# Kernel tuning notes

Hardware: AMD Instinct MI355X
Metric: run time of the kernel (lower is better)

Reference implementation:

```python
import jax, jax.numpy as jnp
import numpy as np

D_MODEL = 768
NHEAD = 12
D_K = D_MODEL // NHEAD
D_FF = 3072
EPS = 1e-6


def layer_norm(x, a, b):
    # torch LayerNorm here: mean/std over last dim, std is UNBIASED (n-1), eps added to std
    n = x.shape[-1]
    m = jnp.mean(x, axis=-1, keepdims=True)
    var = jnp.sum((x - m) ** 2, axis=-1, keepdims=True) / (n - 1)
    return a * (x - m) / (jnp.sqrt(var) + EPS) + b


def setup_inputs() -> dict:
    key = jax.random.key(0)
    ks = jax.random.split(key, 12)
    B, S = 2, 2048
    s = 1.0 / np.sqrt(D_MODEL)
    inp = {
        'x': jax.random.normal(ks[0], (B, S, D_MODEL), jnp.float32),
        'mask': jnp.ones((B, 1, S), jnp.int32),
        'Wq': jax.random.normal(ks[1], (D_MODEL, D_MODEL), jnp.float32) * s,
        'bq': jnp.zeros((D_MODEL,), jnp.float32),
        'Wk': jax.random.normal(ks[2], (D_MODEL, D_MODEL), jnp.float32) * s,
        'bk': jnp.zeros((D_MODEL,), jnp.float32),
        'Wv': jax.random.normal(ks[3], (D_MODEL, D_MODEL), jnp.float32) * s,
        'bv': jnp.zeros((D_MODEL,), jnp.float32),
        'Wo': jax.random.normal(ks[4], (D_MODEL, D_MODEL), jnp.float32) * s,
        'bo': jnp.zeros((D_MODEL,), jnp.float32),
        'ln1_a': jnp.ones((D_MODEL,), jnp.float32),
        'ln1_b': jnp.zeros((D_MODEL,), jnp.float32),
        'W1': jax.random.normal(ks[5], (D_MODEL, D_FF), jnp.float32) * s,
        'b1': jnp.zeros((D_FF,), jnp.float32),
        'W2': jax.random.normal(ks[6], (D_FF, D_MODEL), jnp.float32) * (1.0 / np.sqrt(D_FF)),
        'b2': jnp.zeros((D_MODEL,), jnp.float32),
        'ln2_a': jnp.ones((D_MODEL,), jnp.float32),
        'ln2_b': jnp.zeros((D_MODEL,), jnp.float32),
    }
    return inp


def reference(x, mask, Wq, bq, Wk, bk, Wv, bv, Wo, bo, ln1_a, ln1_b, W1, b1, W2, b2, ln2_a, ln2_b):
    B, S, _ = x.shape
    # --- sublayer 1: pre-norm self-attention + residual (dropout = eval/no-op) ---
    h = layer_norm(x, ln1_a, ln1_b)
    q = (h @ Wq + bq).reshape(B, S, NHEAD, D_K).transpose(0, 2, 1, 3)  # [B,H,S,Dk]
    k = (h @ Wk + bk).reshape(B, S, NHEAD, D_K).transpose(0, 2, 1, 3)
    v = (h @ Wv + bv).reshape(B, S, NHEAD, D_K).transpose(0, 2, 1, 3)
    scores = jnp.einsum('bhqd,bhkd->bhqk', q, k) / np.sqrt(D_K)  # [B,H,S,S]
    scores = jnp.where(mask[:, None] == 0, jnp.float32(-1e9), scores)
    attn = jax.nn.softmax(scores, axis=-1)
    ctx = jnp.einsum('bhqk,bhkd->bhqd', attn, v)  # [B,H,S,Dk]
    ctx = ctx.transpose(0, 2, 1, 3).reshape(B, S, D_MODEL)
    x = x + (ctx @ Wo + bo)
    # --- sublayer 2: pre-norm FFN + residual ---
    h2 = layer_norm(x, ln2_a, ln2_b)
    ff = jax.nn.relu(h2 @ W1 + b1) @ W2 + b2
    return x + ff
```

## Files before the change

kernel.cpp:

```cpp
#include <hip/hip_runtime.h>
#include <hip/hip_bf16.h>
#include <stdint.h>

#define DM 768
#define DFF 3072
#define NH 12
#define DK 64
#define SS 2048
#define NTOK 4096
#define KCH 2

typedef __hip_bfloat16 bf16;
typedef short bf16x8 __attribute__((ext_vector_type(8)));
typedef float f32x4 __attribute__((ext_vector_type(4)));

#define MFMA16(a, b, c) __builtin_amdgcn_mfma_f32_16x16x32_bf16((a), (b), (c), 0, 0, 0)

#define QSCALE 0.18033688011112042f

#if __has_builtin(__builtin_amdgcn_exp2f)
#define EXP2F(x) __builtin_amdgcn_exp2f(x)
#else
#define EXP2F(x) exp2f(x)
#endif

static __device__ __forceinline__ bf16 f2b(float f) { return __float2bfloat16(f); }
static __device__ __forceinline__ unsigned short f2b_bits(float f) {
    bf16 h = __float2bfloat16(f);
    return *reinterpret_cast<unsigned short*>(&h);
}
static __device__ __forceinline__ float b2f(bf16 h) { return __bfloat162float(h); }

static __device__ __forceinline__ void g2l16(const void* g, void* l) {
    __builtin_amdgcn_global_load_lds(
        (const __attribute__((address_space(1))) unsigned int*)g,
        (__attribute__((address_space(3))) unsigned int*)(uintptr_t)l,
        16, 0, 0);
}

__global__ __launch_bounds__(256) void transpose_all(const float* Wq, const float* Wk,
                                                     const float* Wv, const float* Wo,
                                                     const float* W1, const float* W2,
                                                     bf16* WqT, bf16* WkT, bf16* WvT,
                                                     bf16* WoT, bf16* W1T, bf16* W2T) {
    __shared__ float tile[32][33];
    int id = blockIdx.x;
    const float* W; bf16* WT; int K, N, n0, k0;
    if (id < 2304) {
        int z = id / 576, r = id % 576;
        W  = (z == 0) ? Wq : (z == 1) ? Wk : (z == 2) ? Wv : Wo;
        WT = (z == 0) ? WqT : (z == 1) ? WkT : (z == 2) ? WvT : WoT;
        K = 768; N = 768; n0 = (r % 24) * 32; k0 = (r / 24) * 32;
    } else if (id < 4608) {
        int r = id - 2304; W = W1; WT = W1T;
        K = 768; N = 3072; n0 = (r % 96) * 32; k0 = (r / 96) * 32;
    } else {
        int r = id - 4608; W = W2; WT = W2T;
        K = 3072; N = 768; n0 = (r % 24) * 32; k0 = (r / 24) * 32;
    }
    int tx = threadIdx.x & 31, ty = threadIdx.x >> 5;
#pragma unroll
    for (int r = ty; r < 32; r += 8)
        tile[r][tx] = W[(size_t)(k0 + r) * N + n0 + tx];
    __syncthreads();
#pragma unroll
    for (int r = ty; r < 32; r += 8)
        WT[(size_t)(n0 + r) * K + k0 + tx] = f2b(tile[tx][r]);
}

__global__ __launch_bounds__(256) void ln_fwd(const float* __restrict__ x,
                                              const float* __restrict__ g,
                                              const float* __restrict__ be,
                                              bf16* __restrict__ out) {
    int wid = threadIdx.x >> 6, lane = threadIdx.x & 63;
    int row = blockIdx.x * 4 + wid;
    const float* xr = x + (size_t)row * DM;
    float v[12];
    float s = 0.f;
#pragma unroll
    for (int i = 0; i < 12; ++i) { v[i] = xr[lane + i * 64]; s += v[i]; }
#pragma unroll
    for (int off = 32; off >= 1; off >>= 1) s += __shfl_xor(s, off);
    float mean = s * (1.f / 768.f);
    float s2 = 0.f;
#pragma unroll
    for (int i = 0; i < 12; ++i) { float d = v[i] - mean; s2 += d * d; }
#pragma unroll
    for (int off = 32; off >= 1; off >>= 1) s2 += __shfl_xor(s2, off);
    float rstd = 1.f / (sqrtf(s2 * (1.f / 767.f)) + 1e-6f);
    bf16* orow = out + (size_t)row * DM;
#pragma unroll
    for (int i = 0; i < 12; ++i) {
        int c = lane + i * 64;
        orow[c] = f2b(g[c] * (v[i] - mean) * rstd + be[c]);
    }
}

__device__ __forceinline__ void gemm_core(const bf16* __restrict__ A,
                                          const bf16* __restrict__ BT,
                                          int K, int bm, int bn,
                                          bf16* As, bf16* Bs,
                                          f32x4 acc[4][4]) {
    int tid = threadIdx.x;
    int lane = tid & 63, quad = lane >> 4, lid = lane & 15;
    int wid = tid >> 6;
    int wm = (wid >> 1) * 64, wn = (wid & 1) * 64;
    int s0 = tid, s1 = tid + 256;
    int r0 = s0 >> 2, c0 = (s0 & 3) ^ ((r0 >> 1) & 3);
    int r1 = s1 >> 2, c1 = (s1 & 3) ^ ((r1 >> 1) & 3);
    const bf16* A0 = A + (size_t)(bm + r0) * K + c0 * 8;
    const bf16* A1 = A + (size_t)(bm + r1) * K + c1 * 8;
    const bf16* B0 = BT + (size_t)(bn + r0) * K + c0 * 8;
    const bf16* B1 = BT + (size_t)(bn + r1) * K + c1 * 8;
    int rdc = quad ^ ((lid >> 1) & 3);
    g2l16(A0, As + s0 * 8);
    g2l16(B0, Bs + s0 * 8);
    g2l16(A1, As + s1 * 8);
    g2l16(B1, Bs + s1 * 8);
    for (int k0 = 0; k0 < K; k0 += 32) {
        __syncthreads();
        int cur = (k0 >> 5) & 1;
        if (k0 + 32 < K) {
            int nb = (cur ^ 1) * 4096;
            g2l16(A0 + k0 + 32, As + nb + s0 * 8);
            g2l16(B0 + k0 + 32, Bs + nb + s0 * 8);
            g2l16(A1 + k0 + 32, As + nb + s1 * 8);
            g2l16(B1 + k0 + 32, Bs + nb + s1 * 8);
        }
        const bf16* Ac = As + cur * 4096;
        const bf16* Bc = Bs + cur * 4096;
        bf16x8 af[4], bfr[4];
#pragma unroll
        for (int i = 0; i < 4; ++i) af[i]  = *(const bf16x8*)&Ac[(wm + i * 16 + lid) * 32 + rdc * 8];
#pragma unroll
        for (int j = 0; j < 4; ++j) bfr[j] = *(const bf16x8*)&Bc[(wn + j * 16 + lid) * 32 + rdc * 8];
#pragma unroll
        for (int i = 0; i < 4; ++i)
#pragma unroll
            for (int j = 0; j < 4; ++j)
                acc[i][j] = MFMA16(af[i], bfr[j], acc[i][j]);
    }
}

__global__ __launch_bounds__(256) void gemm_qkv(const bf16* __restrict__ A,
                                                const bf16* __restrict__ WqT,
                                                const bf16* __restrict__ WkT,
                                                const bf16* __restrict__ WvT,
                                                const float* __restrict__ bq,
                                                const float* __restrict__ bk,
                                                const float* __restrict__ bv,
                                                bf16* __restrict__ qb,
                                                bf16* __restrict__ kb,
                                                bf16* __restrict__ vtb) {
    __shared__ bf16 As[2 * 128 * 32];
    __shared__ bf16 Bs[2 * 128 * 32];
    int which = blockIdx.x / 6;
    int bn = (blockIdx.x % 6) * 128;
    int bm = blockIdx.y * 128;
    const bf16* BT = (which == 0) ? WqT : (which == 1) ? WkT : WvT;
    const float* bias = (which == 0) ? bq : (which == 1) ? bk : bv;
    f32x4 acc[4][4] = {};
    gemm_core(A, BT, DM, bm, bn, As, Bs, acc);

    int tid = threadIdx.x, wid = tid >> 6, lane = tid & 63, quad = lane >> 4, lid = lane & 15;
    int wm = (wid >> 1) * 64, wn = (wid & 1) * 64;
    float sc = (which == 0) ? QSCALE : 1.f;
#pragma unroll
    for (int j = 0; j < 4; ++j) {
        int col = bn + wn + j * 16 + lid;
        float bb = bias[col];
        int hh = col >> 6, d = col & 63;
#pragma unroll
        for (int i = 0; i < 4; ++i) {
            int rowbase = bm + wm + i * 16 + quad * 4;
            int b = rowbase >> 11;
            int s0 = rowbase & 2047;
            if (which == 2) {
                ushort4 pk;
                pk.x = f2b_bits(acc[i][j][0] + bb);
                pk.y = f2b_bits(acc[i][j][1] + bb);
                pk.z = f2b_bits(acc[i][j][2] + bb);
                pk.w = f2b_bits(acc[i][j][3] + bb);
                *(ushort4*)&vtb[(((size_t)b * NH + hh) * DK + d) * SS + s0] = pk;
            } else {
                bf16* dst = which ? kb : qb;
#pragma unroll
                for (int r = 0; r < 4; ++r)
                    dst[(((size_t)b * NH + hh) * SS + (s0 + r)) * DK + d] = f2b((acc[i][j][r] + bb) * sc);
            }
        }
    }
}

template <int EPI>
__global__ __launch_bounds__(256) void gemm_ep(const bf16* __restrict__ A,
                                               const bf16* __restrict__ BT,
                                               const float* __restrict__ bias,
                                               const float* __restrict__ res,
                                               void* __restrict__ outp,
                                               int N, int K) {
    __shared__ bf16 As[2 * 128 * 32];
    __shared__ bf16 Bs[2 * 128 * 32];
    int bm = blockIdx.y * 128, bn = blockIdx.x * 128;
    f32x4 acc[4][4] = {};
    gemm_core(A, BT, K, bm, bn, As, Bs, acc);

    int tid = threadIdx.x, wid = tid >> 6, lane = tid & 63, quad = lane >> 4, lid = lane & 15;
    int wm = (wid >> 1) * 64, wn = (wid & 1) * 64;
#pragma unroll
    for (int j = 0; j < 4; ++j) {
        int col = bn + wn + j * 16 + lid;
        float bb = bias[col];
#pragma unroll
        for (int i = 0; i < 4; ++i) {
#pragma unroll
            for (int r = 0; r < 4; ++r) {
                int row = bm + wm + i * 16 + quad * 4 + r;
                float v = acc[i][j][r] + bb;
                if (EPI == 2) {
                    ((float*)outp)[(size_t)row * N + col] = res[(size_t)row * N + col] + v;
                } else {
                    ((bf16*)outp)[(size_t)row * N + col] = f2b(fmaxf(v, 0.f));
                }
            }
        }
    }
}

template <int EPI>
__global__ __launch_bounds__(256) void gemm_ep64(const bf16* __restrict__ A,
                                                 const bf16* __restrict__ BT,
                                                 const float* __restrict__ bias,
                                                 const float* __restrict__ res,
                                                 void* __restrict__ outp,
                                                 int N, int K) {
    __shared__ bf16 As[2 * 64 * 32];
    __shared__ bf16 Bs[2 * 128 * 32];
    int bm = blockIdx.y * 64, bn = blockIdx.x * 128;
    int tid = threadIdx.x, wid = tid >> 6, lane = tid & 63, quad = lane >> 4, lid = lane & 15;
    int wm = (wid >> 1) * 32, wn = (wid & 1) * 64;
    f32x4 acc[2][4] = {};
    int ra = tid >> 2, ca = (tid & 3) ^ ((ra >> 1) & 3);
    int s0 = tid, s1 = tid + 256;
    int rb0 = s0 >> 2, cb0 = (s0 & 3) ^ ((rb0 >> 1) & 3);
    int rb1 = s1 >> 2, cb1 = (s1 & 3) ^ ((rb1 >> 1) & 3);
    const bf16* Ap = A + (size_t)(bm + ra) * K + ca * 8;
    const bf16* B0 = BT + (size_t)(bn + rb0) * K + cb0 * 8;
    const bf16* B1 = BT + (size_t)(bn + rb1) * K + cb1 * 8;
    int rdc = quad ^ ((lid >> 1) & 3);
    g2l16(Ap, As + tid * 8);
    g2l16(B0, Bs + s0 * 8);
    g2l16(B1, Bs + s1 * 8);
    for (int k0 = 0; k0 < K; k0 += 32) {
        __syncthreads();
        int cur = (k0 >> 5) & 1;
        if (k0 + 32 < K) {
            g2l16(Ap + k0 + 32, As + (cur ^ 1) * 2048 + tid * 8);
            g2l16(B0 + k0 + 32, Bs + (cur ^ 1) * 4096 + s0 * 8);
            g2l16(B1 + k0 + 32, Bs + (cur ^ 1) * 4096 + s1 * 8);
        }
        const bf16* Ac = As + cur * 2048;
        const bf16* Bc = Bs + cur * 4096;
        bf16x8 af[2], bfr[4];
#pragma unroll
        for (int i = 0; i < 2; ++i) af[i]  = *(const bf16x8*)&Ac[(wm + i * 16 + lid) * 32 + rdc * 8];
#pragma unroll
        for (int j = 0; j < 4; ++j) bfr[j] = *(const bf16x8*)&Bc[(wn + j * 16 + lid) * 32 + rdc * 8];
#pragma unroll
        for (int i = 0; i < 2; ++i)
#pragma unroll
            for (int j = 0; j < 4; ++j)
                acc[i][j] = MFMA16(af[i], bfr[j], acc[i][j]);
    }
#pragma unroll
    for (int j = 0; j < 4; ++j) {
        int col = bn + wn + j * 16 + lid;
        float bb = bias[col];
#pragma unroll
        for (int i = 0; i < 2; ++i) {
#pragma unroll
            for (int r = 0; r < 4; ++r) {
                int row = bm + wm + i * 16 + quad * 4 + r;
                float v = acc[i][j][r] + bb;
                if (EPI == 2) {
                    ((float*)outp)[(size_t)row * N + col] = res[(size_t)row * N + col] + v;
                } else {
                    ((bf16*)outp)[(size_t)row * N + col] = f2b(fmaxf(v, 0.f));
                }
            }
        }
    }
}

__global__ __launch_bounds__(256) void attn_part(const bf16* __restrict__ qb,
                                                 const bf16* __restrict__ kb,
                                                 const bf16* __restrict__ vtb,
                                                 const int* __restrict__ mask,
                                                 bf16* __restrict__ part,
                                                 float* __restrict__ lws) {
    __shared__ bf16 Ks[64 * 64];
    __shared__ bf16 VTs[64 * 64];
    __shared__ bf16 Ps[64 * 72];
    int bh = blockIdx.y;
    int b = bh / NH;
    int q0 = blockIdx.x * 64;
    int kc = blockIdx.z;
    const bf16* Kp = kb  + (size_t)bh * SS * DK;
    const bf16* VT = vtb + (size_t)bh * DK * SS;
    int tid = threadIdx.x, wid = tid >> 6, lane = tid & 63, quad = lane >> 4, lid = lane & 15;

    int s0 = tid, s1 = tid + 256;
    int r0 = s0 >> 3, c0 = (s0 & 7) ^ (r0 & 7);
    int r1 = s1 >> 3, c1 = (s1 & 7) ^ (r1 & 7);

    const bf16* Qrow = qb + ((size_t)bh * SS + q0 + wid * 16 + lid) * DK;
    bf16x8 qf0 = *(const bf16x8*)&Qrow[quad * 8];
    bf16x8 qf1 = *(const bf16x8*)&Qrow[32 + quad * 8];

    bf16x8 ones;
#pragma unroll
    for (int i = 0; i < 8; ++i) ones[i] = (short)0x3F80;

    int rdc  = quad ^ (lid & 7);
    int rdc2 = rdc ^ 4;
    const int* mrow = mask + b * SS;

    f32x4 accv[4] = {};
    f32x4 accl = {};

    for (int t = kc * (SS / 64 / KCH); t < (kc + 1) * (SS / 64 / KCH); ++t) {
        int k0 = t * 64;
        __syncthreads();
        g2l16(Kp + (size_t)(k0 + r0) * DK + c0 * 8, Ks + s0 * 8);
        g2l16(Kp + (size_t)(k0 + r1) * DK + c1 * 8, Ks + s1 * 8);
        g2l16(VT + (size_t)r0 * SS + k0 + c0 * 8, VTs + s0 * 8);
        g2l16(VT + (size_t)r1 * SS + k0 + c1 * 8, VTs + s1 * 8);
        __syncthreads();

#pragma unroll
        for (int ns = 0; ns < 4; ++ns) {
            bf16x8 kf0 = *(const bf16x8*)&Ks[(ns * 16 + lid) * 64 + rdc * 8];
            bf16x8 kf1 = *(const bf16x8*)&Ks[(ns * 16 + lid) * 64 + rdc2 * 8];
            f32x4 st = {};
            st = MFMA16(kf0, qf0, st);
            st = MFMA16(kf1, qf1, st);
            int4 mk = *(const int4*)&mrow[k0 + ns * 16 + quad * 4];
            float p0 = mk.x ? EXP2F(st[0]) : 0.f;
            float p1 = mk.y ? EXP2F(st[1]) : 0.f;
            float p2 = mk.z ? EXP2F(st[2]) : 0.f;
            float p3 = mk.w ? EXP2F(st[3]) : 0.f;
            __hip_bfloat162 h01 = __float22bfloat162_rn(make_float2(p0, p1));
            __hip_bfloat162 h23 = __float22bfloat162_rn(make_float2(p2, p3));
            uint2 pw;
            pw.x = *(unsigned int*)&h01;
            pw.y = *(unsigned int*)&h23;
            *(uint2*)&Ps[(wid * 16 + lid) * 72 + ns * 16 + quad * 4] = pw;
        }

        bf16x8 pa0 = *(const bf16x8*)&Ps[(wid * 16 + lid) * 72 + quad * 8];
        bf16x8 pa1 = *(const bf16x8*)&Ps[(wid * 16 + lid) * 72 + 32 + quad * 8];

        accl = MFMA16(pa0, ones, accl);
        accl = MFMA16(pa1, ones, accl);

#pragma unroll
        for (int ds = 0; ds < 4; ++ds) {
            bf16x8 vf0 = *(const bf16x8*)&VTs[(ds * 16 + lid) * 64 + rdc * 8];
            bf16x8 vf1 = *(const bf16x8*)&VTs[(ds * 16 + lid) * 64 + rdc2 * 8];
            accv[ds] = MFMA16(pa0, vf0, accv[ds]);
            accv[ds] = MFMA16(pa1, vf1, accv[ds]);
        }
    }

    if (lid == 0) {
#pragma unroll
        for (int r = 0; r < 4; ++r)
            lws[((size_t)kc * (2 * NH) + bh) * SS + q0 + wid * 16 + quad * 4 + r] = accl[r];
    }

    bf16* pb = part + ((size_t)kc * (2 * NH) + bh) * DK * SS;
    int qbase = q0 + wid * 16 + quad * 4;
#pragma unroll
    for (int ds = 0; ds < 4; ++ds) {
        int d = ds * 16 + lid;
        ushort4 pk;
        pk.x = f2b_bits(accv[ds][0]);
        pk.y = f2b_bits(accv[ds][1]);
        pk.z = f2b_bits(accv[ds][2]);
        pk.w = f2b_bits(accv[ds][3]);
        *(ushort4*)&pb[(size_t)d * SS + qbase] = pk;
    }
}

__global__ __launch_bounds__(256) void attn_combine(const bf16* __restrict__ part,
                                                    const float* __restrict__ lws,
                                                    bf16* __restrict__ ctx) {
    __shared__ float tile[64][66];
    __shared__ float linv[64];
    int bh = blockIdx.y;
    int b = bh / NH, h = bh % NH;
    int q0 = blockIdx.x * 64;
    int tid = threadIdx.x;

    if (tid < 64) {
        float l = 0.f;
#pragma unroll
        for (int kc = 0; kc < KCH; ++kc)
            l += lws[((size_t)kc * (2 * NH) + bh) * SS + q0 + tid];
        linv[tid] = 1.f / l;
    }

    int d = tid >> 2, qs = (tid & 3) * 16;
    const bf16* p0 = part + (((size_t)0 * (2 * NH) + bh) * DK + d) * SS + q0 + qs;
    const bf16* p1 = part + (((size_t)1 * (2 * NH) + bh) * DK + d) * SS + q0 + qs;
    bf16x8 a0 = *(const bf16x8*)p0;
    bf16x8 a1 = *(const bf16x8*)(p0 + 8);
    bf16x8 b0 = *(const bf16x8*)p1;
    bf16x8 b1 = *(const bf16x8*)(p1 + 8);
#pragma unroll
    for (int i = 0; i < 8; ++i) {
        tile[d][qs + i]     = b2f(((const bf16*)&a0)[i]) + b2f(((const bf16*)&b0)[i]);
        tile[d][qs + 8 + i] = b2f(((const bf16*)&a1)[i]) + b2f(((const bf16*)&b1)[i]);
    }
    __syncthreads();

    int q = tid >> 2, ds2 = (tid & 3) * 16;
    float rl = linv[q];
    unsigned int wv[8];
#pragma unroll
    for (int i = 0; i < 8; ++i) {
        __hip_bfloat162 hh = __float22bfloat162_rn(
            make_float2(tile[ds2 + 2 * i][q] * rl, tile[ds2 + 2 * i + 1][q] * rl));
        wv[i] = *(unsigned int*)&hh;
    }
    bf16* crow = ctx + (size_t)(b * SS + q0 + q) * DM + h * DK + ds2;
    uint4 u0 = {wv[0], wv[1], wv[2], wv[3]};
    uint4 u1 = {wv[4], wv[5], wv[6], wv[7]};
    *(uint4*)&crow[0] = u0;
    *(uint4*)&crow[8] = u1;
}

extern "C" void kernel_launch(void* const* d_in, const int* in_sizes, int n_in,
                              void* d_out, int out_size, void* d_ws, size_t ws_size,
                              hipStream_t stream) {
    const float* x    = (const float*)d_in[0];
    const int*   mask = (const int*)d_in[1];
    const float* Wq   = (const float*)d_in[2];
    const float* bq   = (const float*)d_in[3];
    const float* Wk   = (const float*)d_in[4];
    const float* bk   = (const float*)d_in[5];
    const float* Wv   = (const float*)d_in[6];
    const float* bv   = (const float*)d_in[7];
    const float* Wo   = (const float*)d_in[8];
    const float* bo   = (const float*)d_in[9];
    const float* ln1a = (const float*)d_in[10];
    const float* ln1b = (const float*)d_in[11];
    const float* W1   = (const float*)d_in[12];
    const float* b1   = (const float*)d_in[13];
    const float* W2   = (const float*)d_in[14];
    const float* b2   = (const float*)d_in[15];
    const float* ln2a = (const float*)d_in[16];
    const float* ln2b = (const float*)d_in[17];
    float* out = (float*)d_out;

    char* w = (char*)d_ws;
    bf16* h   = (bf16*)w; w += (size_t)NTOK * DM * 2;
    bf16* qb  = (bf16*)w; w += (size_t)NTOK * DM * 2;
    bf16* kb  = (bf16*)w; w += (size_t)NTOK * DM * 2;
    bf16* vtb = (bf16*)w; w += (size_t)NTOK * DM * 2;
    bf16* ctx = (bf16*)w; w += (size_t)NTOK * DM * 2;
    bf16* h2  = (bf16*)w; w += (size_t)NTOK * DM * 2;
    bf16* ffa = (bf16*)w; w += (size_t)NTOK * DFF * 2;
    float* x1 = (float*)w; w += (size_t)NTOK * DM * 4;
    bf16* WqT = (bf16*)w; w += (size_t)DM * DM * 2;
    bf16* WkT = (bf16*)w; w += (size_t)DM * DM * 2;
    bf16* WvT = (bf16*)w; w += (size_t)DM * DM * 2;
    bf16* WoT = (bf16*)w; w += (size_t)DM * DM * 2;
    bf16* W1T = (bf16*)w; w += (size_t)DM * DFF * 2;
    bf16* W2T = (bf16*)w; w += (size_t)DM * DFF * 2;

    bf16*  part = ffa;
    float* lws  = x1;

    transpose_all<<<6912, 256, 0, stream>>>(Wq, Wk, Wv, Wo, W1, W2,
                                            WqT, WkT, WvT, WoT, W1T, W2T);

    ln_fwd<<<NTOK / 4, 256, 0, stream>>>(x, ln1a, ln1b, h);
    gemm_qkv<<<dim3(18, 32), 256, 0, stream>>>(h, WqT, WkT, WvT, bq, bk, bv, qb, kb, vtb);
    attn_part<<<dim3(SS / 64, 2 * NH, KCH), 256, 0, stream>>>(qb, kb, vtb, mask, part, lws);
    attn_combine<<<dim3(SS / 64, 2 * NH), 256, 0, stream>>>(part, lws, ctx);
    gemm_ep64<2><<<dim3(6, 64), 256, 0, stream>>>(ctx, WoT, bo, x, (void*)x1, DM, DM);
    ln_fwd<<<NTOK / 4, 256, 0, stream>>>(x1, ln2a, ln2b, h2);
    gemm_ep<3><<<dim3(24, 32), 256, 0, stream>>>(h2, W1T, b1, nullptr, (void*)ffa, DFF, DM);
    gemm_ep64<2><<<dim3(6, 64), 256, 0, stream>>>(ffa, W2T, b2, x1, (void*)out, DM, DFF);
}
```

Baseline: 296.8 us.

## Switch attention partial kernel to 32x32x16 MFMA with 2x2 wave tiling

Rewrites the attention partial kernel so each wave computes a 32x32 score tile (key half by query half) and a 32x32 output tile (query half by head-dim half) using 32x32x16 bf16 MFMA instead of per-wave 16-row strips with 16x16x32 MFMA. The row-sum is now accumulated in scalar registers and reduced through LDS instead of an extra MFMA against a ones vector. A block barrier is added between writing P and consuming it, since waves now read P rows produced by other waves. Launch bounds request 6 blocks per CU. The aim is fewer LDS fragment reads per MFMA and better MFMA efficiency, at the cost of an extra barrier per tile and different register pressure.

```diff
diff --git a/kernel.cpp b/kernel.cpp
--- a/kernel.cpp
+++ b/kernel.cpp
@@ -13,8 +13,10 @@
 typedef __hip_bfloat16 bf16;
 typedef short bf16x8 __attribute__((ext_vector_type(8)));
 typedef float f32x4 __attribute__((ext_vector_type(4)));
+typedef float f32x16 __attribute__((ext_vector_type(16)));
 
 #define MFMA16(a, b, c) __builtin_amdgcn_mfma_f32_16x16x32_bf16((a), (b), (c), 0, 0, 0)
+#define MFMA32(a, b, c) __builtin_amdgcn_mfma_f32_32x32x16_bf16((a), (b), (c), 0, 0, 0)
 
 #define QSCALE 0.18033688011112042f
 
@@ -292,12 +294,12 @@
     }
 }
 
-__global__ __launch_bounds__(256) void attn_part(const bf16* __restrict__ qb,
-                                                 const bf16* __restrict__ kb,
-                                                 const bf16* __restrict__ vtb,
-                                                 const int* __restrict__ mask,
-                                                 bf16* __restrict__ part,
-                                                 float* __restrict__ lws) {
+__global__ __launch_bounds__(256, 6) void attn_part(const bf16* __restrict__ qb,
+                                                    const bf16* __restrict__ kb,
+                                                    const bf16* __restrict__ vtb,
+                                                    const int* __restrict__ mask,
+                                                    bf16* __restrict__ part,
+                                                    float* __restrict__ lws) {
     __shared__ bf16 Ks[64 * 64];
     __shared__ bf16 VTs[64 * 64];
     __shared__ bf16 Ps[64 * 72];
@@ -307,26 +309,26 @@
     int kc = blockIdx.z;
     const bf16* Kp = kb  + (size_t)bh * SS * DK;
     const bf16* VT = vtb + (size_t)bh * DK * SS;
-    int tid = threadIdx.x, wid = tid >> 6, lane = tid & 63, quad = lane >> 4, lid = lane & 15;
+    int tid = threadIdx.x, wid = tid >> 6, lane = tid & 63;
+    int l5 = lane & 31, h = lane >> 5;
 
     int s0 = tid, s1 = tid + 256;
     int r0 = s0 >> 3, c0 = (s0 & 7) ^ (r0 & 7);
     int r1 = s1 >> 3, c1 = (s1 & 7) ^ (r1 & 7);
 
-    const bf16* Qrow = qb + ((size_t)bh * SS + q0 + wid * 16 + lid) * DK;
-    bf16x8 qf0 = *(const bf16x8*)&Qrow[quad * 8];
-    bf16x8 qf1 = *(const bf16x8*)&Qrow[32 + quad * 8];
-
-    bf16x8 ones;
-#pragma unroll
-    for (int i = 0; i < 8; ++i) ones[i] = (short)0x3F80;
-
-    int rdc  = quad ^ (lid & 7);
-    int rdc2 = rdc ^ 4;
+    int kq = (wid & 1) * 32, qq = (wid >> 1) * 32;
+    int qh = (wid & 1) * 32, dh = (wid >> 1) * 32;
+
+    const bf16* Qrow = qb + ((size_t)bh * SS + q0 + qq + l5) * DK + h * 8;
+    bf16x8 qf[4];
+#pragma unroll
+    for (int kst = 0; kst < 4; ++kst) qf[kst] = *(const bf16x8*)&Qrow[kst * 16];
+
     const int* mrow = mask + b * SS;
-
-    f32x4 accv[4] = {};
-    f32x4 accl = {};
+    int swz = l5 & 7;
+
+    f32x16 accv = {};
+    float lp = 0.f;
 
     for (int t = kc * (SS / 64 / KCH); t < (kc + 1) * (SS / 64 / KCH); ++t) {
         int k0 = t * 64;
@@ -337,58 +339,57 @@
         g2l16(VT + (size_t)r1 * SS + k0 + c1 * 8, VTs + s1 * 8);
         __syncthreads();
 
-#pragma unroll
-        for (int ns = 0; ns < 4; ++ns) {
-            bf16x8 kf0 = *(const bf16x8*)&Ks[(ns * 16 + lid) * 64 + rdc * 8];
-            bf16x8 kf1 = *(const bf16x8*)&Ks[(ns * 16 + lid) * 64 + rdc2 * 8];
-            f32x4 st = {};
-            st = MFMA16(kf0, qf0, st);
-            st = MFMA16(kf1, qf1, st);
-            int4 mk = *(const int4*)&mrow[k0 + ns * 16 + quad * 4];
-            float p0 = mk.x ? EXP2F(st[0]) : 0.f;
-            float p1 = mk.y ? EXP2F(st[1]) : 0.f;
-            float p2 = mk.z ? EXP2F(st[2]) : 0.f;
-            float p3 = mk.w ? EXP2F(st[3]) : 0.f;
+        f32x16 st = {};
+#pragma unroll
+        for (int kst = 0; kst < 4; ++kst) {
+            bf16x8 kf = *(const bf16x8*)&Ks[(kq + l5) * 64 + ((2 * kst + h) ^ swz) * 8];
+            st = MFMA32(kf, qf[kst], st);
+        }
+#pragma unroll
+        for (int g = 0; g < 4; ++g) {
+            int4 mk = *(const int4*)&mrow[k0 + kq + 8 * g + 4 * h];
+            float p0 = mk.x ? EXP2F(st[4 * g + 0]) : 0.f;
+            float p1 = mk.y ? EXP2F(st[4 * g + 1]) : 0.f;
+            float p2 = mk.z ? EXP2F(st[4 * g + 2]) : 0.f;
+            float p3 = mk.w ? EXP2F(st[4 * g + 3]) : 0.f;
+            lp += (p0 + p1) + (p2 + p3);
             __hip_bfloat162 h01 = __float22bfloat162_rn(make_float2(p0, p1));
             __hip_bfloat162 h23 = __float22bfloat162_rn(make_float2(p2, p3));
             uint2 pw;
             pw.x = *(unsigned int*)&h01;
             pw.y = *(unsigned int*)&h23;
-            *(uint2*)&Ps[(wid * 16 + lid) * 72 + ns * 16 + quad * 4] = pw;
-        }
-
-        bf16x8 pa0 = *(const bf16x8*)&Ps[(wid * 16 + lid) * 72 + quad * 8];
-        bf16x8 pa1 = *(const bf16x8*)&Ps[(wid * 16 + lid) * 72 + 32 + quad * 8];
-
-        accl = MFMA16(pa0, ones, accl);
-        accl = MFMA16(pa1, ones, accl);
-
-#pragma unroll
-        for (int ds = 0; ds < 4; ++ds) {
-            bf16x8 vf0 = *(const bf16x8*)&VTs[(ds * 16 + lid) * 64 + rdc * 8];
-            bf16x8 vf1 = *(const bf16x8*)&VTs[(ds * 16 + lid) * 64 + rdc2 * 8];
-            accv[ds] = MFMA16(pa0, vf0, accv[ds]);
-            accv[ds] = MFMA16(pa1, vf1, accv[ds]);
-        }
-    }
-
-    if (lid == 0) {
-#pragma unroll
-        for (int r = 0; r < 4; ++r)
-            lws[((size_t)kc * (2 * NH) + bh) * SS + q0 + wid * 16 + quad * 4 + r] = accl[r];
+            *(uint2*)&Ps[(qq + l5) * 72 + kq + 8 * g + 4 * h] = pw;
+        }
+        __syncthreads();
+
+#pragma unroll
+        for (int kst = 0; kst < 4; ++kst) {
+            bf16x8 pa = *(const bf16x8*)&Ps[(qh + l5) * 72 + kst * 16 + h * 8];
+            bf16x8 vf = *(const bf16x8*)&VTs[(dh + l5) * 64 + ((2 * kst + h) ^ swz) * 8];
+            accv = MFMA32(pa, vf, accv);
+        }
+    }
+
+    lp += __shfl_xor(lp, 32);
+    __syncthreads();
+    float* lred = (float*)Ks;
+    if (lane < 32) lred[wid * 32 + l5] = lp;
+    __syncthreads();
+    if (tid < 64) {
+        int base = (tid >> 5) * 2;
+        float l = lred[base * 32 + (tid & 31)] + lred[(base + 1) * 32 + (tid & 31)];
+        lws[((size_t)kc * (2 * NH) + bh) * SS + q0 + tid] = l;
     }
 
     bf16* pb = part + ((size_t)kc * (2 * NH) + bh) * DK * SS;
-    int qbase = q0 + wid * 16 + quad * 4;
-#pragma unroll
-    for (int ds = 0; ds < 4; ++ds) {
-        int d = ds * 16 + lid;
+#pragma unroll
+    for (int g = 0; g < 4; ++g) {
         ushort4 pk;
-        pk.x = f2b_bits(accv[ds][0]);
-        pk.y = f2b_bits(accv[ds][1]);
-        pk.z = f2b_bits(accv[ds][2]);
-        pk.w = f2b_bits(accv[ds][3]);
-        *(ushort4*)&pb[(size_t)d * SS + qbase] = pk;
+        pk.x = f2b_bits(accv[4 * g + 0]);
+        pk.y = f2b_bits(accv[4 * g + 1]);
+        pk.z = f2b_bits(accv[4 * g + 2]);
+        pk.w = f2b_bits(accv[4 * g + 3]);
+        *(ushort4*)&pb[(size_t)(dh + l5) * SS + q0 + qh + 8 * g + 4 * h] = pk;
     }
 }
 
```

Measured after the change: 328.8 us. +10.8%, slower.
